# Performance work log

Hardware: AMD Instinct MI355X
Metric: run time of the kernel (lower is better)

## Reference

```python
import jax, jax.numpy as jnp
import numpy as np

IN_ = 64
FEATURE = 1024
BATCH = 256

def setup_inputs() -> dict:
    key = jax.random.key(0)
    kx, kw = jax.random.split(key)
    x = jax.random.normal(kx, (BATCH, IN_, FEATURE), dtype=jnp.float32)
    # W[i] corresponds to torch Linear weight of shape [out_features, in_features]
    # scaled like torch's default kaiming-uniform-ish init (bound = 1/sqrt(fan_in))
    bound = 1.0 / np.sqrt(FEATURE)
    W = jax.random.uniform(kw, (IN_, FEATURE, FEATURE), dtype=jnp.float32,
                           minval=-bound, maxval=bound)
    return {"x": x, "W": W}

def reference(x, W):
    # Per-position independent linear: out[b,i,o] = sum_f x[b,i,f] * W[i,o,f]
    # (torch Linear computes x @ W^T). Single batched GEMM via einsum.
    return jnp.einsum('bif,iof->bio', x, W)
```

## Files before the change

kernel.cpp:

```cpp
#include <hip/hip_runtime.h>
#include <hip/hip_bf16.h>

#define IN_CNT 64
#define FEAT   1024
#define BATCH  256

#define BM 256
#define BN 256
#define BK 32
#define KT (FEAT / BK)

typedef __attribute__((ext_vector_type(4))) float f32x4;
typedef __attribute__((ext_vector_type(8))) short bf16x8;

__device__ __forceinline__ short f2bf(float f) {
    __hip_bfloat16 h = __float2bfloat16(f);
    return __builtin_bit_cast(short, h);
}

__device__ __forceinline__ bf16x8 pack8(f32x4 a, f32x4 b) {
    bf16x8 v;
    v[0] = f2bf(a[0]); v[1] = f2bf(a[1]); v[2] = f2bf(a[2]); v[3] = f2bf(a[3]);
    v[4] = f2bf(b[0]); v[5] = f2bf(b[1]); v[6] = f2bf(b[2]); v[7] = f2bf(b[3]);
    return v;
}

__device__ __forceinline__ void barrier_lgkm() {
    asm volatile("s_waitcnt lgkmcnt(0)" ::: "memory");
    __builtin_amdgcn_s_barrier();
    asm volatile("" ::: "memory");
}

__device__ __forceinline__ void gload16(const float* g, float* l) {
    __builtin_amdgcn_global_load_lds(
        (const __attribute__((address_space(1))) void*)g,
        (__attribute__((address_space(3))) void*)l, 16, 0, 0);
}

__global__ __launch_bounds__(512, 2)
void split_linear_kernel(const float* __restrict__ x,
                         const float* __restrict__ W,
                         float* __restrict__ out)
{
    __shared__ __align__(16) float lds[32768];

    const int tid = threadIdx.x;

    const int bid = blockIdx.x;
    const int swz = ((bid & 7) << 5) | (bid >> 3);
    const int gi   = swz >> 2;
    const int ncol = (swz & 3) << 8;

    const int lane = tid & 63;
    const int wid  = tid >> 6;
    const int wm   = wid >> 2;
    const int wn   = wid & 3;
    const int lr   = lane & 15;
    const int lh   = lane >> 4;

    const int lrow = lane >> 3;
    const int lgr  = (lane & 7) ^ lrow;
    const float* Asrc = x + ((size_t)lrow * IN_CNT + gi) * FEAT + lgr * 4;
    const float* Bsrc = W + ((size_t)gi * FEAT + ncol + lrow) * FEAT + lgr * 4;

    f32x4 acc[8][4];
#pragma unroll
    for (int m = 0; m < 8; ++m)
#pragma unroll
        for (int n = 0; n < 4; ++n)
            acc[m][n] = (f32x4){0.f, 0.f, 0.f, 0.f};

    auto STAGE_A = [&](int kt, int bb) {
        float* base = lds + bb * 16384;
        const float* a0 = Asrc + (size_t)kt * BK;
#pragma unroll
        for (int i = 0; i < 4; ++i) {
            const int c = wid * 4 + i;
            gload16(a0 + (size_t)c * (8 * IN_CNT * FEAT), base + c * 256);
        }
    };
    auto STAGE_B = [&](int kt, int bb) {
        float* base = lds + bb * 16384 + 8192;
        const float* b0 = Bsrc + (size_t)kt * BK;
#pragma unroll
        for (int i = 0; i < 4; ++i) {
            const int c = wid * 4 + i;
            gload16(b0 + (size_t)c * (8 * FEAT), base + c * 256);
        }
    };

    const int sl0 = ((2 * lh)     ^ (lr & 7)) << 2;
    const int sl1 = ((2 * lh + 1) ^ (lr & 7)) << 2;

    bf16x8 bfr[4];
    auto READ_B = [&](int bb) {
        const float* bufB = lds + bb * 16384 + 8192;
#pragma unroll
        for (int nf = 0; nf < 4; ++nf) {
            const float* rp = bufB + (wn * 64 + nf * 16 + lr) * 32;
            bfr[nf] = pack8(*(const f32x4*)(rp + sl0), *(const f32x4*)(rp + sl1));
        }
    };
    auto MFMA_HALF = [&](int bb, int ph) {
        const float* bufA = lds + bb * 16384;
#pragma unroll
        for (int m4 = 0; m4 < 4; ++m4) {
            const int mf = ph * 4 + m4;
            const float* rp = bufA + (wm * 128 + mf * 16 + lr) * 32;
            bf16x8 af = pack8(*(const f32x4*)(rp + sl0), *(const f32x4*)(rp + sl1));
#pragma unroll
            for (int nf = 0; nf < 4; ++nf)
                acc[mf][nf] = __builtin_amdgcn_mfma_f32_16x16x32_bf16(
                    af, bfr[nf], acc[mf][nf], 0, 0, 0);
        }
    };

    STAGE_B(0, 0);
    STAGE_A(0, 0);
    STAGE_B(1, 1);
    asm volatile("s_waitcnt vmcnt(4)" ::: "memory");
    __builtin_amdgcn_s_barrier();
    asm volatile("" ::: "memory");

    for (int t = 0; t < KT; ++t) {
        const int bb = t & 1;
        READ_B(bb);
        if (t + 1 < KT) STAGE_A(t + 1, bb ^ 1);
        __builtin_amdgcn_s_setprio(1);
        MFMA_HALF(bb, 0);
        __builtin_amdgcn_s_setprio(0);
        barrier_lgkm();
        if (t + 2 < KT) STAGE_B(t + 2, bb);
        __builtin_amdgcn_s_setprio(1);
        MFMA_HALF(bb, 1);
        __builtin_amdgcn_s_setprio(0);
        if (t + 2 < KT) {
            asm volatile("s_waitcnt vmcnt(4)" ::: "memory");
        } else {
            asm volatile("s_waitcnt vmcnt(0)" ::: "memory");
        }
        __builtin_amdgcn_s_barrier();
        asm volatile("" ::: "memory");
    }

#define ELD 260
    float* elds = lds;
#pragma unroll
    for (int s = 0; s < 4; ++s) {
        barrier_lgkm();
        if (wm == (s >> 1)) {
            const int mfb = (s & 1) * 4;
#pragma unroll
            for (int f = 0; f < 4; ++f)
#pragma unroll
                for (int nf = 0; nf < 4; ++nf)
#pragma unroll
                    for (int j = 0; j < 4; ++j)
                        elds[(f * 16 + lh * 4 + j) * ELD + wn * 64 + nf * 16 + lr]
                            = acc[mfb + f][nf][j];
        }
        barrier_lgkm();
#pragma unroll
        for (int rr = 0; rr < 8; ++rr) {
            const int rowl = wid * 8 + rr;
            f32x4 v = *(const f32x4*)&elds[rowl * ELD + lane * 4];
            const int m = s * 64 + rowl;
            *(f32x4*)&out[((size_t)m * IN_CNT + gi) * FEAT + ncol + lane * 4] = v;
        }
    }
#undef ELD
}

extern "C" void kernel_launch(void* const* d_in, const int* in_sizes, int n_in,
                              void* d_out, int out_size, void* d_ws, size_t ws_size,
                              hipStream_t stream) {
    const float* x   = (const float*)d_in[0];
    const float* W   = (const float*)d_in[1];
    float*       out = (float*)d_out;

    dim3 grid(IN_CNT * (FEAT / BN));
    dim3 block(512);
    hipLaunchKernelGGL(split_linear_kernel, grid, block, 0, stream, x, W, out);
}
```

Before: 94.19 us.

## Halve N tile, stage A as bf16 via registers, triple-buffer B

Cuts the block tile from 256x256 to 256x128 with 256 threads, doubling grid size. The x tile is now loaded into registers, converted to bf16 once, and written to a swizzled LDS buffer. Each wave no longer repacks fp32 A from LDS per MFMA, which removes redundant conversions and LDS traffic. W tiles use a three-slot DMA ring, so each k-step needs only one barrier. In exchange, W reuse per block drops, x is re-read by twice as many blocks, and register pressure from the A staging registers rises.

Measured after the change: 99.62 us. +5.8%, slower.

```diff
diff --git a/kernel.cpp b/kernel.cpp
--- a/kernel.cpp
+++ b/kernel.cpp
@@ -6,7 +6,7 @@
 #define BATCH  256
 
 #define BM 256
-#define BN 256
+#define BN 128
 #define BK 32
 #define KT (FEAT / BK)
 
@@ -37,32 +37,40 @@
         (__attribute__((address_space(3))) void*)l, 16, 0, 0);
 }
 
-__global__ __launch_bounds__(512, 2)
+__global__ __launch_bounds__(256, 2)
 void split_linear_kernel(const float* __restrict__ x,
                          const float* __restrict__ W,
                          float* __restrict__ out)
 {
-    __shared__ __align__(16) float lds[32768];
+    __shared__ __align__(16) char smem[81920];
+    short* Alds = (short*)smem;
+    float* Blds = (float*)(smem + 32768);
+    float* elds = (float*)smem;
 
     const int tid = threadIdx.x;
 
     const int bid = blockIdx.x;
-    const int swz = ((bid & 7) << 5) | (bid >> 3);
-    const int gi   = swz >> 2;
-    const int ncol = (swz & 3) << 8;
+    const int swz = ((bid & 7) << 6) | (bid >> 3);
+    const int gi   = swz >> 3;
+    const int ncol = (swz & 7) << 7;
 
     const int lane = tid & 63;
     const int wid  = tid >> 6;
-    const int wm   = wid >> 2;
-    const int wn   = wid & 3;
+    const int wm   = wid >> 1;
+    const int wn   = wid & 1;
     const int lr   = lane & 15;
     const int lh   = lane >> 4;
 
+    const int sq   = tid & 7;
+    const int asr0 = tid >> 3;
+    const int arow = (asr0 << 1) + (sq >> 2);
+    const float* Aglob = x + ((size_t)arow * IN_CNT + gi) * FEAT + (sq & 3) * 8;
+
     const int lrow = lane >> 3;
     const int lgr  = (lane & 7) ^ lrow;
-    const float* Asrc = x + ((size_t)lrow * IN_CNT + gi) * FEAT + lgr * 4;
     const float* Bsrc = W + ((size_t)gi * FEAT + ncol + lrow) * FEAT + lgr * 4;
 
+    f32x4 aA[4][2];
     f32x4 acc[8][4];
 #pragma unroll
     for (int m = 0; m < 8; ++m)
@@ -70,17 +78,24 @@
         for (int n = 0; n < 4; ++n)
             acc[m][n] = (f32x4){0.f, 0.f, 0.f, 0.f};
 
-    auto STAGE_A = [&](int kt, int bb) {
-        float* base = lds + bb * 16384;
-        const float* a0 = Asrc + (size_t)kt * BK;
+    auto LOAD_A = [&](int kt) {
 #pragma unroll
-        for (int i = 0; i < 4; ++i) {
-            const int c = wid * 4 + i;
-            gload16(a0 + (size_t)c * (8 * IN_CNT * FEAT), base + c * 256);
+        for (int p = 0; p < 4; ++p) {
+            const float* q = Aglob + (size_t)p * (64 * IN_CNT * FEAT) + (size_t)kt * BK;
+            aA[p][0] = *(const f32x4*)q;
+            aA[p][1] = *(const f32x4*)(q + 4);
         }
     };
-    auto STAGE_B = [&](int kt, int bb) {
-        float* base = lds + bb * 16384 + 8192;
+    auto WRITE_A = [&](int ab) {
+        short* base = Alds + ab * 8192;
+#pragma unroll
+        for (int p = 0; p < 4; ++p) {
+            const int sr = asr0 + p * 32;
+            *(bf16x8*)&base[sr * 64 + ((sq ^ (sr & 7)) << 3)] = pack8(aA[p][0], aA[p][1]);
+        }
+    };
+    auto DMA_B = [&](int kt, int q) {
+        float* base = Blds + q * 4096;
         const float* b0 = Bsrc + (size_t)kt * BK;
 #pragma unroll
         for (int i = 0; i < 4; ++i) {
@@ -89,51 +104,48 @@
         }
     };
 
-    const int sl0 = ((2 * lh)     ^ (lr & 7)) << 2;
-    const int sl1 = ((2 * lh + 1) ^ (lr & 7)) << 2;
+    const int bsl0 = ((2 * lh)     ^ (lr & 7)) << 2;
+    const int bsl1 = ((2 * lh + 1) ^ (lr & 7)) << 2;
 
-    bf16x8 bfr[4];
-    auto READ_B = [&](int bb) {
-        const float* bufB = lds + bb * 16384 + 8192;
+    auto COMPUTE = [&](int ab, int q) {
+        const float* bufB = Blds + q * 4096;
+        const short* bufA = Alds + ab * 8192;
+        bf16x8 bfr[4];
 #pragma unroll
         for (int nf = 0; nf < 4; ++nf) {
             const float* rp = bufB + (wn * 64 + nf * 16 + lr) * 32;
-            bfr[nf] = pack8(*(const f32x4*)(rp + sl0), *(const f32x4*)(rp + sl1));
+            bfr[nf] = pack8(*(const f32x4*)(rp + bsl0), *(const f32x4*)(rp + bsl1));
         }
-    };
-    auto MFMA_HALF = [&](int bb, int ph) {
-        const float* bufA = lds + bb * 16384;
+        __builtin_amdgcn_s_setprio(1);
 #pragma unroll
-        for (int m4 = 0; m4 < 4; ++m4) {
-            const int mf = ph * 4 + m4;
-            const float* rp = bufA + (wm * 128 + mf * 16 + lr) * 32;
-            bf16x8 af = pack8(*(const f32x4*)(rp + sl0), *(const f32x4*)(rp + sl1));
+        for (int mf = 0; mf < 8; ++mf) {
+            const int r  = wm * 128 + mf * 16 + lr;
+            const int sr = r >> 1;
+            bf16x8 af = *(const bf16x8*)&bufA[sr * 64
+                            + (((((r & 1) << 2) + lh) ^ (sr & 7)) << 3)];
 #pragma unroll
             for (int nf = 0; nf < 4; ++nf)
                 acc[mf][nf] = __builtin_amdgcn_mfma_f32_16x16x32_bf16(
                     af, bfr[nf], acc[mf][nf], 0, 0, 0);
         }
+        __builtin_amdgcn_s_setprio(0);
     };
 
-    STAGE_B(0, 0);
-    STAGE_A(0, 0);
-    STAGE_B(1, 1);
+    DMA_B(0, 0);
+    DMA_B(1, 1);
+    LOAD_A(0);
+    WRITE_A(0);
     asm volatile("s_waitcnt vmcnt(4)" ::: "memory");
     __builtin_amdgcn_s_barrier();
     asm volatile("" ::: "memory");
 
+    int q0 = 0, q1 = 1, q2 = 2;
+    int ab = 0;
     for (int t = 0; t < KT; ++t) {
-        const int bb = t & 1;
-        READ_B(bb);
-        if (t + 1 < KT) STAGE_A(t + 1, bb ^ 1);
-        __builtin_amdgcn_s_setprio(1);
-        MFMA_HALF(bb, 0);
-        __builtin_amdgcn_s_setprio(0);
-        barrier_lgkm();
-        if (t + 2 < KT) STAGE_B(t + 2, bb);
-        __builtin_amdgcn_s_setprio(1);
-        MFMA_HALF(bb, 1);
-        __builtin_amdgcn_s_setprio(0);
+        if (t + 1 < KT) LOAD_A(t + 1);
+        if (t + 2 < KT) DMA_B(t + 2, q2);
+        COMPUTE(ab, q0);
+        if (t + 1 < KT) WRITE_A(ab ^ 1);
         if (t + 2 < KT) {
             asm volatile("s_waitcnt vmcnt(4)" ::: "memory");
         } else {
@@ -141,10 +153,11 @@
         }
         __builtin_amdgcn_s_barrier();
         asm volatile("" ::: "memory");
+        const int tq = q0; q0 = q1; q1 = q2; q2 = tq;
+        ab ^= 1;
     }
 
-#define ELD 260
-    float* elds = lds;
+#define ELD 132
 #pragma unroll
     for (int s = 0; s < 4; ++s) {
         barrier_lgkm();
@@ -162,10 +175,10 @@
         barrier_lgkm();
 #pragma unroll
         for (int rr = 0; rr < 8; ++rr) {
-            const int rowl = wid * 8 + rr;
-            f32x4 v = *(const f32x4*)&elds[rowl * ELD + lane * 4];
+            const int rowl = wid * 16 + rr * 2 + (lane >> 5);
+            f32x4 v = *(const f32x4*)&elds[rowl * ELD + (lane & 31) * 4];
             const int m = s * 64 + rowl;
-            *(f32x4*)&out[((size_t)m * IN_CNT + gi) * FEAT + ncol + lane * 4] = v;
+            *(f32x4*)&out[((size_t)m * IN_CNT + gi) * FEAT + ncol + (lane & 31) * 4] = v;
         }
     }
 #undef ELD
@@ -179,6 +192,6 @@
     float*       out = (float*)d_out;
 
     dim3 grid(IN_CNT * (FEAT / BN));
-    dim3 block(512);
+    dim3 block(256);
     hipLaunchKernelGGL(split_linear_kernel, grid, block, 0, stream, x, W, out);
 }
```
